# Performance work log

Hardware: AMD Instinct MI355X
Metric: run time of the kernel (lower is better)

The kernel has to match this reference:

```python
import jax, jax.numpy as jnp
import numpy as np

NEG_SLOPE = 0.2


def gat_conv(x, src, dst, W, a_src, a_dst, bias, concat, num_nodes):
    # x: [N, F_in]; W: [F_in, H*C]; a_src/a_dst: [H, C]
    H, C = a_src.shape
    h = (x @ W).reshape(num_nodes, H, C)               # [N,H,C]
    alpha_s = jnp.sum(h * a_src[None], axis=-1)        # [N,H]
    alpha_d = jnp.sum(h * a_dst[None], axis=-1)        # [N,H]
    e = jax.nn.leaky_relu(alpha_s[src] + alpha_d[dst], NEG_SLOPE)  # [E,H]
    m = jax.ops.segment_max(e, dst, num_segments=num_nodes)
    m = jnp.where(jnp.isfinite(m), m, 0.0)
    ex = jnp.exp(e - m[dst])
    denom = jax.ops.segment_sum(ex, dst, num_segments=num_nodes)
    alpha = ex / (denom[dst] + 1e-16)                  # scatter-softmax over dst
    msg = h[src] * alpha[:, :, None]                   # [E,H,C]
    out = jax.ops.segment_sum(msg, dst, num_segments=num_nodes)  # [N,H,C]
    if concat:
        out = out.reshape(num_nodes, H * C)
    else:
        out = out.mean(axis=1)
    return out + bias


def setup_inputs() -> dict:
    key = jax.random.key(0)
    ks = jax.random.split(key, 12)
    N, E = 50000, 800000
    num_concat, F_in, hid, H1, H2, n_cls = 2, 128, 64, 4, 1, 16
    x_list = jax.random.normal(ks[0], (num_concat, N, F_in), dtype=jnp.float32)
    edge_index = jax.random.randint(ks[1], (2, E), 0, N, dtype=jnp.int64)
    s = 0.1
    W1 = jax.random.normal(ks[2], (num_concat, F_in, H1 * hid), dtype=jnp.float32) * s
    att_src1 = jax.random.normal(ks[3], (num_concat, H1, hid), dtype=jnp.float32) * s
    att_dst1 = jax.random.normal(ks[4], (num_concat, H1, hid), dtype=jnp.float32) * s
    bias1 = jnp.zeros((num_concat, H1 * hid), dtype=jnp.float32)
    W2 = jax.random.normal(ks[5], (hid * H1 * num_concat, H2 * n_cls), dtype=jnp.float32) * s
    att_src2 = jax.random.normal(ks[6], (H2, n_cls), dtype=jnp.float32) * s
    att_dst2 = jax.random.normal(ks[7], (H2, n_cls), dtype=jnp.float32) * s
    bias2 = jnp.zeros((n_cls,), dtype=jnp.float32)
    return {"x_list": x_list, "edge_index": edge_index,
            "W1": W1, "att_src1": att_src1, "att_dst1": att_dst1, "bias1": bias1,
            "W2": W2, "att_src2": att_src2, "att_dst2": att_dst2, "bias2": bias2}


def reference(x_list, edge_index, W1, att_src1, att_dst1, bias1, W2, att_src2, att_dst2, bias2):
    num_concat, N, _ = x_list.shape
    loop = jnp.arange(N, dtype=edge_index.dtype)
    src = jnp.concatenate([edge_index[0], loop])  # PyG add_self_loops=True
    dst = jnp.concatenate([edge_index[1], loop])
    hidden = [jax.nn.elu(gat_conv(x_list[k], src, dst, W1[k], att_src1[k], att_dst1[k],
                                  bias1[k], True, N))
              for k in range(num_concat)]
    x = jnp.concatenate(hidden, axis=-1)           # [N, hid*H1*num_concat]
    out = gat_conv(x, src, dst, W2, att_src2, att_dst2, bias2, False, N)
    return out
```

## Files before the change

kernel.cpp:

```cpp
#include <hip/hip_runtime.h>

#define LEAKY(v) ((v) >= 0.0f ? (v) : 0.2f * (v))

typedef __attribute__((ext_vector_type(8))) short bf16x8;
typedef __attribute__((ext_vector_type(4))) float f32x4;

__device__ __forceinline__ unsigned short f2bf(float f) {
    unsigned int u = __float_as_uint(f);
    unsigned int r = u + 0x7FFFu + ((u >> 16) & 1u);
    return (unsigned short)(r >> 16);
}
__device__ __forceinline__ float bf2f(unsigned short u) {
    return __uint_as_float(((unsigned int)u) << 16);
}
__device__ __forceinline__ unsigned int pk2(float a, float b) {
    return (unsigned int)f2bf(a) | ((unsigned int)f2bf(b) << 16);
}


__global__ __launch_bounds__(256) void count_deg(const int* ei, int* deg, int E, int Etot) {
    int i = blockIdx.x * 256 + threadIdx.x;
    if (i >= Etot) return;
    int d = (i < E) ? ei[E + i] : (i - E);
    atomicAdd(&deg[d], 1);
}

__global__ __launch_bounds__(512) void scan_block(const int* deg, int* excl, int* bsum, int n) {
    __shared__ int s[512];
    int t = threadIdx.x;
    int i = blockIdx.x * 512 + t;
    int v = (i < n) ? deg[i] : 0;
    s[t] = v;
    __syncthreads();
    for (int d = 1; d < 512; d <<= 1) {
        int x = 0;
        if (t >= d) x = s[t - d];
        __syncthreads();
        if (t >= d) s[t] += x;
        __syncthreads();
    }
    if (i < n) excl[i] = s[t] - v;
    if (t == 511) bsum[blockIdx.x] = s[511];
}

__global__ __launch_bounds__(512) void scan_sums(const int* bsum, int* boff, int nb) {
    __shared__ int s[512];
    int t = threadIdx.x;
    int v = (t < nb) ? bsum[t] : 0;
    s[t] = v;
    __syncthreads();
    for (int d = 1; d < 512; d <<= 1) {
        int x = 0;
        if (t >= d) x = s[t - d];
        __syncthreads();
        if (t >= d) s[t] += x;
        __syncthreads();
    }
    boff[t] = s[t] - v;
}

__global__ __launch_bounds__(256) void finalize_off(int* csr, int* cursor, const int* boff, int n, int etot) {
    int i = blockIdx.x * 256 + threadIdx.x;
    if (i < n) {
        int v = csr[i] + boff[i >> 9];
        csr[i] = v;
        cursor[i] = v;
    }
    if (i == 0) csr[n] = etot;
}

__global__ __launch_bounds__(256) void scatter_edge(const int* ei, int* cursor, int* srcs, int* dsts,
                                                    int E, int Etot) {
    int i = blockIdx.x * 256 + threadIdx.x;
    if (i >= Etot) return;
    int s, d;
    if (i < E) { s = ei[i]; d = ei[E + i]; }
    else       { s = i - E; d = s; }
    int pos = atomicAdd(&cursor[d], 1);
    srcs[pos] = s;
    dsts[pos] = d;
}


__global__ __launch_bounds__(256) void xpack(const float* __restrict__ x, unsigned short* __restrict__ xp,
                                             int nrows) {
    int id = blockIdx.x * 256 + threadIdx.x;
    if (id >= nrows * 16) return;
    int row = id >> 4, q = id & 15;
    const float* src = x + (size_t)row * 128 + q * 8;
    float4 a = *(const float4*)src;
    float4 b = *(const float4*)(src + 4);
    uint4 v;
    v.x = pk2(a.x, a.y); v.y = pk2(a.z, a.w);
    v.z = pk2(b.x, b.y); v.w = pk2(b.z, b.w);
    *(uint4*)(xp + (size_t)row * 128 + ((q ^ (row & 7)) << 3)) = v;
}

__global__ __launch_bounds__(256) void wpack1(const float* __restrict__ W1, unsigned short* __restrict__ wt1) {
    int id = blockIdx.x * 256 + threadIdx.x;
    if (id >= 8192) return;
    int conv = id >> 12, rem = id & 4095;
    int c = rem >> 4, q = rem & 15;
    const float* src = W1 + (size_t)conv * 32768 + (size_t)(q * 8) * 256 + c;
    float w[8];
#pragma unroll
    for (int j = 0; j < 8; ++j) w[j] = src[j * 256];
    uint4 v;
    v.x = pk2(w[0], w[1]); v.y = pk2(w[2], w[3]);
    v.z = pk2(w[4], w[5]); v.w = pk2(w[6], w[7]);
    *(uint4*)(wt1 + (size_t)conv * 32768 + c * 128 + ((q ^ (c & 7)) << 3)) = v;
}

__global__ __launch_bounds__(256) void wpack2(const float* __restrict__ W2, unsigned short* __restrict__ wt2) {
    int id = blockIdx.x * 256 + threadIdx.x;
    if (id >= 1024) return;
    int s = id >> 6, l = id & 63;
    const float* src = W2 + (size_t)(s * 32 + (l >> 4) * 8) * 16 + (l & 15);
    float w[8];
#pragma unroll
    for (int j = 0; j < 8; ++j) w[j] = src[j * 16];
    uint4 v;
    v.x = pk2(w[0], w[1]); v.y = pk2(w[2], w[3]);
    v.z = pk2(w[4], w[5]); v.w = pk2(w[6], w[7]);
    *(uint4*)(wt2 + (size_t)id * 8) = v;
}


__global__ __launch_bounds__(256) void gemm1_mfma(const unsigned short* __restrict__ xp,
                                                  const unsigned short* __restrict__ wt1,
                                                  const float* __restrict__ asw, const float* __restrict__ adw,
                                                  unsigned short* __restrict__ hp,
                                                  float* __restrict__ as1, float* __restrict__ ad1, int N) {
    __shared__ unsigned short As[64 * 128];
    __shared__ unsigned short Ws[256 * 128];
    int conv = blockIdx.y;
    int t = threadIdx.x;
    int w = t >> 6, l = t & 63;

    const uint4* xsrc = (const uint4*)(xp + ((size_t)conv * N + (size_t)blockIdx.x * 64) * 128);
#pragma unroll
    for (int p = 0; p < 4; ++p) {
        int id = p * 256 + t;
        int row = id >> 4;
        int grow = blockIdx.x * 64 + row;
        uint4 v = make_uint4(0, 0, 0, 0);
        if (grow < N) v = xsrc[id];
        *(uint4*)(As + (size_t)id * 8) = v;
    }
    const uint4* wsrc = (const uint4*)(wt1 + (size_t)conv * 32768);
#pragma unroll
    for (int p = 0; p < 16; ++p) {
        int id = p * 256 + t;
        *(uint4*)(Ws + (size_t)id * 8) = wsrc[id];
    }
    __syncthreads();

    f32x4 acc[4][4];
#pragma unroll
    for (int mt = 0; mt < 4; ++mt)
#pragma unroll
        for (int nt = 0; nt < 4; ++nt) acc[mt][nt] = (f32x4){0.f, 0.f, 0.f, 0.f};

    int lr = l & 15, lg = l >> 4;
#pragma unroll
    for (int s = 0; s < 4; ++s) {
        int kq = s * 4 + lg;
        bf16x8 af[4], bf[4];
#pragma unroll
        for (int mt = 0; mt < 4; ++mt) {
            int r = mt * 16 + lr;
            af[mt] = *(const bf16x8*)(As + r * 128 + ((kq ^ (r & 7)) << 3));
        }
#pragma unroll
        for (int nt = 0; nt < 4; ++nt) {
            int c = w * 64 + nt * 16 + lr;
            bf[nt] = *(const bf16x8*)(Ws + c * 128 + ((kq ^ (c & 7)) << 3));
        }
#pragma unroll
        for (int mt = 0; mt < 4; ++mt)
#pragma unroll
            for (int nt = 0; nt < 4; ++nt)
                acc[mt][nt] = __builtin_amdgcn_mfma_f32_16x16x32_bf16(af[mt], bf[nt], acc[mt][nt], 0, 0, 0);
    }

    float aswv[4], adwv[4];
#pragma unroll
    for (int nt = 0; nt < 4; ++nt) {
        aswv[nt] = asw[conv * 256 + w * 64 + nt * 16 + lr];
        adwv[nt] = adw[conv * 256 + w * 64 + nt * 16 + lr];
    }
#pragma unroll
    for (int mt = 0; mt < 4; ++mt) {
#pragma unroll
        for (int i = 0; i < 4; ++i) {
            int grow = blockIdx.x * 64 + mt * 16 + lg * 4 + i;
            bool ok = grow < N;
            float sv = 0.f, dv = 0.f;
#pragma unroll
            for (int nt = 0; nt < 4; ++nt) {
                float hv = acc[mt][nt][i];
                if (ok) hp[(size_t)grow * 512 + (nt * 16 + lr) * 8 + conv * 4 + w] = f2bf(hv);
                sv += hv * aswv[nt];
                dv += hv * adwv[nt];
            }
#pragma unroll
            for (int o = 1; o < 16; o <<= 1) {
                sv += __shfl_xor(sv, o);
                dv += __shfl_xor(dv, o);
            }
            if (lr == 0 && ok) {
                as1[(size_t)conv * N * 4 + (size_t)grow * 4 + w] = sv;
                ad1[(size_t)conv * N * 4 + (size_t)grow * 4 + w] = dv;
            }
        }
    }
}


__global__ __launch_bounds__(256) void edge_w1(const int* __restrict__ srcs, const int* __restrict__ dsts,
                                               const float* __restrict__ as, const float* __restrict__ ad,
                                               float* __restrict__ pw, int Etot, int N4) {
    int e = blockIdx.x * 256 + threadIdx.x;
    if (e >= Etot) return;
    int s = srcs[e], d = dsts[e];
    float4 a0 = *(const float4*)(as + (size_t)s * 4);
    float4 b0 = *(const float4*)(ad + (size_t)d * 4);
    float4 a1 = *(const float4*)(as + N4 + (size_t)s * 4);
    float4 b1 = *(const float4*)(ad + N4 + (size_t)d * 4);
    float4 p0, p1;
    p0.x = __expf(LEAKY(a0.x + b0.x));
    p0.y = __expf(LEAKY(a0.y + b0.y));
    p0.z = __expf(LEAKY(a0.z + b0.z));
    p0.w = __expf(LEAKY(a0.w + b0.w));
    p1.x = __expf(LEAKY(a1.x + b1.x));
    p1.y = __expf(LEAKY(a1.y + b1.y));
    p1.z = __expf(LEAKY(a1.z + b1.z));
    p1.w = __expf(LEAKY(a1.w + b1.w));
    *(float4*)(pw + (size_t)e * 8)     = p0;
    *(float4*)(pw + (size_t)e * 8 + 4) = p1;
}


#define ACC8(g, pa, pb) {                                                      \
    float h0 = __uint_as_float((g).x << 16), h1 = __uint_as_float((g).x & 0xFFFF0000u); \
    float h2v = __uint_as_float((g).y << 16), h3 = __uint_as_float((g).y & 0xFFFF0000u); \
    float h4 = __uint_as_float((g).z << 16), h5 = __uint_as_float((g).z & 0xFFFF0000u); \
    float h6 = __uint_as_float((g).w << 16), h7 = __uint_as_float((g).w & 0xFFFF0000u); \
    den[0] += (pa).x; acc[0] += (pa).x * h0;                                   \
    den[1] += (pa).y; acc[1] += (pa).y * h1;                                   \
    den[2] += (pa).z; acc[2] += (pa).z * h2v;                                  \
    den[3] += (pa).w; acc[3] += (pa).w * h3;                                   \
    den[4] += (pb).x; acc[4] += (pb).x * h4;                                   \
    den[5] += (pb).y; acc[5] += (pb).y * h5;                                   \
    den[6] += (pb).z; acc[6] += (pb).z * h6;                                   \
    den[7] += (pb).w; acc[7] += (pb).w * h7; }

__global__ __launch_bounds__(256) void agg1_both(const unsigned short* __restrict__ hp,
                                                 const float* __restrict__ pw,
                                                 const int* __restrict__ off, const int* __restrict__ srcs,
                                                 const float* __restrict__ b1,
                                                 unsigned short* __restrict__ x2, int N) {
    int n = blockIdx.x * 4 + (threadIdx.x >> 6);
    int lane = threadIdx.x & 63;
    if (n >= N) return;
    int r0 = off[n], r1 = off[n + 1];

    float acc[8] = {0.f, 0.f, 0.f, 0.f, 0.f, 0.f, 0.f, 0.f};
    float den[8] = {0.f, 0.f, 0.f, 0.f, 0.f, 0.f, 0.f, 0.f};

    for (int base = r0; base < r1; base += 64) {
        int cnt = min(64, r1 - base);
        int my = (base + lane < r1) ? srcs[base + lane] : 0;
        int j = 0;
        for (; j + 2 <= cnt; j += 2) {
            int s0 = __shfl(my, j);
            int s1 = __shfl(my, j + 1);
            uint4 g0 = *(const uint4*)(hp + (size_t)s0 * 512 + lane * 8);
            uint4 g1 = *(const uint4*)(hp + (size_t)s1 * 512 + lane * 8);
            float4 pa0 = *(const float4*)(pw + (size_t)(base + j) * 8);
            float4 pb0 = *(const float4*)(pw + (size_t)(base + j) * 8 + 4);
            float4 pa1 = *(const float4*)(pw + (size_t)(base + j + 1) * 8);
            float4 pb1 = *(const float4*)(pw + (size_t)(base + j + 1) * 8 + 4);
            ACC8(g0, pa0, pb0);
            ACC8(g1, pa1, pb1);
        }
        if (j < cnt) {
            int s0 = __shfl(my, j);
            uint4 g0 = *(const uint4*)(hp + (size_t)s0 * 512 + lane * 8);
            float4 pa0 = *(const float4*)(pw + (size_t)(base + j) * 8);
            float4 pb0 = *(const float4*)(pw + (size_t)(base + j) * 8 + 4);
            ACC8(g0, pa0, pb0);
        }
    }

    unsigned short* xo = x2 + (size_t)n * 512;
#pragma unroll
    for (int q = 0; q < 8; ++q) {
        int k = q >> 2, hd = q & 3;
        int ofs = k * 256 + hd * 64 + lane;
        float o = acc[q] / (den[q] + 1e-16f) + b1[ofs];
        o = o > 0.f ? o : (__expf(o) - 1.0f);
        xo[ofs] = f2bf(o);
    }
}


__global__ __launch_bounds__(256) void gemm2_mfma(const unsigned short* __restrict__ x2,
                                                  const unsigned short* __restrict__ wt2,
                                                  const float* __restrict__ asw2, const float* __restrict__ adw2,
                                                  float* __restrict__ h2,
                                                  float* __restrict__ as2, float* __restrict__ ad2, int N) {
    int t = threadIdx.x;
    int w = t >> 6, l = t & 63;
    int rowbase = (blockIdx.x * 4 + w) * 16;
    if (rowbase >= N) return;
    int lr = l & 15, lg = l >> 4;

    f32x4 acc = (f32x4){0.f, 0.f, 0.f, 0.f};
    const unsigned short* ap = x2 + (size_t)(rowbase + lr) * 512 + lg * 8;
#pragma unroll
    for (int s = 0; s < 16; ++s) {
        bf16x8 av = *(const bf16x8*)(ap + s * 32);
        bf16x8 bv = *(const bf16x8*)(wt2 + ((size_t)s * 64 + l) * 8);
        acc = __builtin_amdgcn_mfma_f32_16x16x32_bf16(av, bv, acc, 0, 0, 0);
    }

    float asv = asw2[lr], adv = adw2[lr];
#pragma unroll
    for (int i = 0; i < 4; ++i) {
        int row = rowbase + lg * 4 + i;
        if (row < N) h2[(size_t)row * 16 + lr] = acc[i];
        float sv = acc[i] * asv, dv = acc[i] * adv;
#pragma unroll
        for (int o = 1; o < 16; o <<= 1) {
            sv += __shfl_xor(sv, o);
            dv += __shfl_xor(dv, o);
        }
        if (lr == 0 && row < N) { as2[row] = sv; ad2[row] = dv; }
    }
}


__global__ __launch_bounds__(256) void edge_w2(const int* __restrict__ srcs, const int* __restrict__ dsts,
                                               const float* __restrict__ as2, const float* __restrict__ ad2,
                                               float* __restrict__ p2, int Etot) {
    int e = blockIdx.x * 256 + threadIdx.x;
    if (e >= Etot) return;
    float v = as2[srcs[e]] + ad2[dsts[e]];
    p2[e] = __expf(LEAKY(v));
}


__global__ __launch_bounds__(256) void agg2(const float* __restrict__ h2,
                                            const float* __restrict__ p2,
                                            const int* __restrict__ off, const int* __restrict__ srcs,
                                            const float* __restrict__ bias2, float* __restrict__ out, int N) {
    int n = blockIdx.x * 4 + (threadIdx.x >> 6);
    int lane = threadIdx.x & 63;
    if (n >= N) return;
    int r0 = off[n], r1 = off[n + 1];

    int c = lane & 15, q = lane >> 4;
    float acc = 0.f, denom = 0.f;
    for (int e = r0 + q; e < r1; e += 4) {
        int s = srcs[e];
        float p = p2[e];
        denom += p;
        acc += p * h2[(size_t)s * 16 + c];
    }
    acc += __shfl_xor(acc, 16);     acc += __shfl_xor(acc, 32);
    denom += __shfl_xor(denom, 16); denom += __shfl_xor(denom, 32);
    if (lane < 16) out[(size_t)n * 16 + c] = acc / (denom + 1e-16f) + bias2[c];
}


extern "C" void kernel_launch(void* const* d_in, const int* in_sizes, int n_in,
                              void* d_out, int out_size, void* d_ws, size_t ws_size,
                              hipStream_t stream) {
    const float* x_list = (const float*)d_in[0];
    const int*   ei     = (const int*)d_in[1];
    const float* W1     = (const float*)d_in[2];
    const float* as1w   = (const float*)d_in[3];
    const float* ad1w   = (const float*)d_in[4];
    const float* b1     = (const float*)d_in[5];
    const float* W2     = (const float*)d_in[6];
    const float* as2w   = (const float*)d_in[7];
    const float* ad2w   = (const float*)d_in[8];
    const float* b2     = (const float*)d_in[9];
    float* out = (float*)d_out;

    const int N = in_sizes[0] / 256;
    const int E = in_sizes[1] / 2;
    const int Etot = E + N;
    const int N4 = N * 4;

    char* ws = (char*)d_ws;
    size_t woff = 0;
    auto alloc = [&](size_t bytes) {
        char* p = ws + woff;
        woff = (woff + bytes + 255) & ~(size_t)255;
        return p;
    };
    int*   csr    = (int*)alloc((size_t)(N + 1) * 4);
    int*   cursor = (int*)alloc((size_t)N * 4);
    int*   srcs   = (int*)alloc((size_t)Etot * 4);
    int*   dsts   = (int*)alloc((size_t)Etot * 4);
    int*   bsum   = (int*)alloc(512 * 4);
    int*   boff   = (int*)alloc(512 * 4);
    float* as1    = (float*)alloc((size_t)N4 * 2 * 4);
    float* ad1    = (float*)alloc((size_t)N4 * 2 * 4);
    float* as2    = (float*)alloc((size_t)N * 4);
    float* ad2    = (float*)alloc((size_t)N * 4);
    unsigned short* xp  = (unsigned short*)alloc((size_t)N * 128 * 2 * 2);
    unsigned short* wt1 = (unsigned short*)alloc(2 * 32768 * 2);
    unsigned short* wt2 = (unsigned short*)alloc(16 * 64 * 8 * 2);
    unsigned short* hp  = (unsigned short*)alloc((size_t)N * 512 * 2);
    unsigned short* x2  = (unsigned short*)alloc((size_t)N * 512 * 2);
    float* h2     = (float*)alloc((size_t)N * 16 * 4);
    float* pw     = (float*)alloc((size_t)Etot * 8 * 4);
    float* p2     = (float*)alloc((size_t)Etot * 4);

    hipMemsetAsync(cursor, 0, (size_t)N * 4, stream);
    int gE = (Etot + 255) / 256;
    count_deg<<<gE, 256, 0, stream>>>(ei, cursor, E, Etot);
    int nb = (N + 511) / 512;
    scan_block<<<nb, 512, 0, stream>>>(cursor, csr, bsum, N);
    scan_sums<<<1, 512, 0, stream>>>(bsum, boff, nb);
    finalize_off<<<(N + 255) / 256, 256, 0, stream>>>(csr, cursor, boff, N, Etot);
    scatter_edge<<<gE, 256, 0, stream>>>(ei, cursor, srcs, dsts, E, Etot);

    for (int k = 0; k < 2; ++k)
        xpack<<<(N * 16 + 255) / 256, 256, 0, stream>>>(x_list + (size_t)k * N * 128,
                                                        xp + (size_t)k * N * 128, N);
    wpack1<<<32, 256, 0, stream>>>(W1, wt1);
    wpack2<<<4, 256, 0, stream>>>(W2, wt2);

    gemm1_mfma<<<dim3((N + 63) / 64, 2), 256, 0, stream>>>(xp, wt1, as1w, ad1w, hp, as1, ad1, N);
    edge_w1<<<gE, 256, 0, stream>>>(srcs, dsts, as1, ad1, pw, Etot, N4);
    agg1_both<<<(N + 3) / 4, 256, 0, stream>>>(hp, pw, csr, srcs, b1, x2, N);

    gemm2_mfma<<<(N + 63) / 64, 256, 0, stream>>>(x2, wt2, as2w, ad2w, h2, as2, ad2, N);
    edge_w2<<<gE, 256, 0, stream>>>(srcs, dsts, as2, ad2, p2, Etot);
    agg2<<<(N + 3) / 4, 256, 0, stream>>>(h2, p2, csr, srcs, b2, out, N);
}
```

Measured before the change: 354.1 us.

## Fuse edge-weight computation into aggregation and bf16 packing into GEMM1

Drops the separate edge_w1/edge_w2 kernels and the per-edge weight buffers (and the dsts array). Attention logits are now recomputed per edge inside the aggregation kernels, using the destination's value held in a register. The x-to-bf16 packing is folded into gemm1's shared-memory load, and the hidden features are re-laid out per conv so that layer-1 aggregation runs as 8 channel slices per node, launched once per conv. This removes large intermediate writes and reads, at the cost of redundant exp computation across slices and more, smaller gathers.

Result: slower. 674.0 us (+90.4%).

```diff
diff --git a/kernel.cpp b/kernel.cpp
--- a/kernel.cpp
+++ b/kernel.cpp
@@ -16,6 +16,8 @@
 __device__ __forceinline__ unsigned int pk2(float a, float b) {
     return (unsigned int)f2bf(a) | ((unsigned int)f2bf(b) << 16);
 }
+__device__ __forceinline__ float lo16(unsigned int u) { return __uint_as_float(u << 16); }
+__device__ __forceinline__ float hi16(unsigned int u) { return __uint_as_float(u & 0xFFFF0000u); }
 
 
 __global__ __launch_bounds__(256) void count_deg(const int* ei, int* deg, int E, int Etot) {
@@ -69,8 +71,7 @@
     if (i == 0) csr[n] = etot;
 }
 
-__global__ __launch_bounds__(256) void scatter_edge(const int* ei, int* cursor, int* srcs, int* dsts,
-                                                    int E, int Etot) {
+__global__ __launch_bounds__(256) void scatter_src(const int* ei, int* cursor, int* srcs, int E, int Etot) {
     int i = blockIdx.x * 256 + threadIdx.x;
     if (i >= Etot) return;
     int s, d;
@@ -78,23 +79,8 @@
     else       { s = i - E; d = s; }
     int pos = atomicAdd(&cursor[d], 1);
     srcs[pos] = s;
-    dsts[pos] = d;
-}
-
-
-__global__ __launch_bounds__(256) void xpack(const float* __restrict__ x, unsigned short* __restrict__ xp,
-                                             int nrows) {
-    int id = blockIdx.x * 256 + threadIdx.x;
-    if (id >= nrows * 16) return;
-    int row = id >> 4, q = id & 15;
-    const float* src = x + (size_t)row * 128 + q * 8;
-    float4 a = *(const float4*)src;
-    float4 b = *(const float4*)(src + 4);
-    uint4 v;
-    v.x = pk2(a.x, a.y); v.y = pk2(a.z, a.w);
-    v.z = pk2(b.x, b.y); v.w = pk2(b.z, b.w);
-    *(uint4*)(xp + (size_t)row * 128 + ((q ^ (row & 7)) << 3)) = v;
-}
+}
+
 
 __global__ __launch_bounds__(256) void wpack1(const float* __restrict__ W1, unsigned short* __restrict__ wt1) {
     int id = blockIdx.x * 256 + threadIdx.x;
@@ -126,7 +112,7 @@
 }
 
 
-__global__ __launch_bounds__(256) void gemm1_mfma(const unsigned short* __restrict__ xp,
+__global__ __launch_bounds__(256) void gemm1_mfma(const float* __restrict__ x_list,
                                                   const unsigned short* __restrict__ wt1,
                                                   const float* __restrict__ asw, const float* __restrict__ adw,
                                                   unsigned short* __restrict__ hp,
@@ -137,15 +123,21 @@
     int t = threadIdx.x;
     int w = t >> 6, l = t & 63;
 
-    const uint4* xsrc = (const uint4*)(xp + ((size_t)conv * N + (size_t)blockIdx.x * 64) * 128);
+    const float* xg = x_list + (size_t)conv * N * 128;
 #pragma unroll
     for (int p = 0; p < 4; ++p) {
         int id = p * 256 + t;
-        int row = id >> 4;
+        int row = id >> 4, q = id & 15;
         int grow = blockIdx.x * 64 + row;
         uint4 v = make_uint4(0, 0, 0, 0);
-        if (grow < N) v = xsrc[id];
-        *(uint4*)(As + (size_t)id * 8) = v;
+        if (grow < N) {
+            const float* src = xg + (size_t)grow * 128 + q * 8;
+            float4 a = *(const float4*)src;
+            float4 b = *(const float4*)(src + 4);
+            v.x = pk2(a.x, a.y); v.y = pk2(a.z, a.w);
+            v.z = pk2(b.x, b.y); v.w = pk2(b.z, b.w);
+        }
+        *(uint4*)(As + row * 128 + ((q ^ (row & 7)) << 3)) = v;
     }
     const uint4* wsrc = (const uint4*)(wt1 + (size_t)conv * 32768);
 #pragma unroll
@@ -199,7 +191,7 @@
 #pragma unroll
             for (int nt = 0; nt < 4; ++nt) {
                 float hv = acc[mt][nt][i];
-                if (ok) hp[(size_t)grow * 512 + (nt * 16 + lr) * 8 + conv * 4 + w] = f2bf(hv);
+                if (ok) hp[((size_t)conv * N + grow) * 256 + (nt * 16 + lr) * 4 + w] = f2bf(hv);
                 sv += hv * aswv[nt];
                 dv += hv * adwv[nt];
             }
@@ -209,98 +201,67 @@
                 dv += __shfl_xor(dv, o);
             }
             if (lr == 0 && ok) {
-                as1[(size_t)conv * N * 4 + (size_t)grow * 4 + w] = sv;
-                ad1[(size_t)conv * N * 4 + (size_t)grow * 4 + w] = dv;
+                as1[((size_t)conv * N + grow) * 4 + w] = sv;
+                ad1[((size_t)conv * N + grow) * 4 + w] = dv;
             }
         }
     }
 }
 
 
-__global__ __launch_bounds__(256) void edge_w1(const int* __restrict__ srcs, const int* __restrict__ dsts,
-                                               const float* __restrict__ as, const float* __restrict__ ad,
-                                               float* __restrict__ pw, int Etot, int N4) {
-    int e = blockIdx.x * 256 + threadIdx.x;
-    if (e >= Etot) return;
-    int s = srcs[e], d = dsts[e];
-    float4 a0 = *(const float4*)(as + (size_t)s * 4);
-    float4 b0 = *(const float4*)(ad + (size_t)d * 4);
-    float4 a1 = *(const float4*)(as + N4 + (size_t)s * 4);
-    float4 b1 = *(const float4*)(ad + N4 + (size_t)d * 4);
-    float4 p0, p1;
-    p0.x = __expf(LEAKY(a0.x + b0.x));
-    p0.y = __expf(LEAKY(a0.y + b0.y));
-    p0.z = __expf(LEAKY(a0.z + b0.z));
-    p0.w = __expf(LEAKY(a0.w + b0.w));
-    p1.x = __expf(LEAKY(a1.x + b1.x));
-    p1.y = __expf(LEAKY(a1.y + b1.y));
-    p1.z = __expf(LEAKY(a1.z + b1.z));
-    p1.w = __expf(LEAKY(a1.w + b1.w));
-    *(float4*)(pw + (size_t)e * 8)     = p0;
-    *(float4*)(pw + (size_t)e * 8 + 4) = p1;
-}
-
-
-#define ACC8(g, pa, pb) {                                                      \
-    float h0 = __uint_as_float((g).x << 16), h1 = __uint_as_float((g).x & 0xFFFF0000u); \
-    float h2v = __uint_as_float((g).y << 16), h3 = __uint_as_float((g).y & 0xFFFF0000u); \
-    float h4 = __uint_as_float((g).z << 16), h5 = __uint_as_float((g).z & 0xFFFF0000u); \
-    float h6 = __uint_as_float((g).w << 16), h7 = __uint_as_float((g).w & 0xFFFF0000u); \
-    den[0] += (pa).x; acc[0] += (pa).x * h0;                                   \
-    den[1] += (pa).y; acc[1] += (pa).y * h1;                                   \
-    den[2] += (pa).z; acc[2] += (pa).z * h2v;                                  \
-    den[3] += (pa).w; acc[3] += (pa).w * h3;                                   \
-    den[4] += (pb).x; acc[4] += (pb).x * h4;                                   \
-    den[5] += (pb).y; acc[5] += (pb).y * h5;                                   \
-    den[6] += (pb).z; acc[6] += (pb).z * h6;                                   \
-    den[7] += (pb).w; acc[7] += (pb).w * h7; }
-
-__global__ __launch_bounds__(256) void agg1_both(const unsigned short* __restrict__ hp,
-                                                 const float* __restrict__ pw,
-                                                 const int* __restrict__ off, const int* __restrict__ srcs,
-                                                 const float* __restrict__ b1,
-                                                 unsigned short* __restrict__ x2, int N) {
-    int n = blockIdx.x * 4 + (threadIdx.x >> 6);
+__global__ __launch_bounds__(256) void agg1_slice(const unsigned short* __restrict__ hpk,
+                                                  const float* __restrict__ as1k, const float* __restrict__ ad1k,
+                                                  const int* __restrict__ off, const int* __restrict__ srcs,
+                                                  const float* __restrict__ b1k,
+                                                  unsigned short* __restrict__ x2, int conv, int N) {
+    int slice = blockIdx.x & 7;
+    int n = (blockIdx.x >> 3) * 4 + (threadIdx.x >> 6);
+    if (n >= N) return;
     int lane = threadIdx.x & 63;
-    if (n >= N) return;
+    int eo = lane >> 2, ci = lane & 3;
     int r0 = off[n], r1 = off[n + 1];
 
+    float4 adn = *(const float4*)(ad1k + (size_t)n * 4);
+
     float acc[8] = {0.f, 0.f, 0.f, 0.f, 0.f, 0.f, 0.f, 0.f};
-    float den[8] = {0.f, 0.f, 0.f, 0.f, 0.f, 0.f, 0.f, 0.f};
-
-    for (int base = r0; base < r1; base += 64) {
-        int cnt = min(64, r1 - base);
-        int my = (base + lane < r1) ? srcs[base + lane] : 0;
-        int j = 0;
-        for (; j + 2 <= cnt; j += 2) {
-            int s0 = __shfl(my, j);
-            int s1 = __shfl(my, j + 1);
-            uint4 g0 = *(const uint4*)(hp + (size_t)s0 * 512 + lane * 8);
-            uint4 g1 = *(const uint4*)(hp + (size_t)s1 * 512 + lane * 8);
-            float4 pa0 = *(const float4*)(pw + (size_t)(base + j) * 8);
-            float4 pb0 = *(const float4*)(pw + (size_t)(base + j) * 8 + 4);
-            float4 pa1 = *(const float4*)(pw + (size_t)(base + j + 1) * 8);
-            float4 pb1 = *(const float4*)(pw + (size_t)(base + j + 1) * 8 + 4);
-            ACC8(g0, pa0, pb0);
-            ACC8(g1, pa1, pb1);
-        }
-        if (j < cnt) {
-            int s0 = __shfl(my, j);
-            uint4 g0 = *(const uint4*)(hp + (size_t)s0 * 512 + lane * 8);
-            float4 pa0 = *(const float4*)(pw + (size_t)(base + j) * 8);
-            float4 pb0 = *(const float4*)(pw + (size_t)(base + j) * 8 + 4);
-            ACC8(g0, pa0, pb0);
-        }
-    }
-
-    unsigned short* xo = x2 + (size_t)n * 512;
-#pragma unroll
-    for (int q = 0; q < 8; ++q) {
-        int k = q >> 2, hd = q & 3;
-        int ofs = k * 256 + hd * 64 + lane;
-        float o = acc[q] / (den[q] + 1e-16f) + b1[ofs];
-        o = o > 0.f ? o : (__expf(o) - 1.0f);
-        xo[ofs] = f2bf(o);
+    float den[4] = {0.f, 0.f, 0.f, 0.f};
+
+    for (int base = r0; base + eo < r1; base += 16) {
+        int e = base + eo;
+        int s = __builtin_nontemporal_load(srcs + e);
+        float4 av = *(const float4*)(as1k + (size_t)s * 4);
+        uint4 g = *(const uint4*)(hpk + (size_t)s * 256 + slice * 32 + ci * 8);
+        float p0 = __expf(LEAKY(av.x + adn.x));
+        float p1 = __expf(LEAKY(av.y + adn.y));
+        float p2 = __expf(LEAKY(av.z + adn.z));
+        float p3 = __expf(LEAKY(av.w + adn.w));
+        den[0] += p0; den[1] += p1; den[2] += p2; den[3] += p3;
+        acc[0] += p0 * lo16(g.x); acc[1] += p1 * hi16(g.x);
+        acc[2] += p2 * lo16(g.y); acc[3] += p3 * hi16(g.y);
+        acc[4] += p0 * lo16(g.z); acc[5] += p1 * hi16(g.z);
+        acc[6] += p2 * lo16(g.w); acc[7] += p3 * hi16(g.w);
+    }
+
+#pragma unroll
+    for (int o = 4; o < 64; o <<= 1) {
+#pragma unroll
+        for (int j = 0; j < 8; ++j) acc[j] += __shfl_xor(acc[j], o);
+#pragma unroll
+        for (int j = 0; j < 4; ++j) den[j] += __shfl_xor(den[j], o);
+    }
+
+    if (eo == 0) {
+        unsigned short* xo = x2 + (size_t)n * 512 + conv * 256;
+#pragma unroll
+        for (int c2 = 0; c2 < 2; ++c2) {
+            int c = slice * 8 + ci * 2 + c2;
+#pragma unroll
+            for (int h = 0; h < 4; ++h) {
+                float o = acc[c2 * 4 + h] / (den[h] + 1e-16f) + b1k[h * 64 + c];
+                o = o > 0.f ? o : (__expf(o) - 1.0f);
+                xo[h * 64 + c] = f2bf(o);
+            }
+        }
     }
 }
 
@@ -341,30 +302,21 @@
 }
 
 
-__global__ __launch_bounds__(256) void edge_w2(const int* __restrict__ srcs, const int* __restrict__ dsts,
-                                               const float* __restrict__ as2, const float* __restrict__ ad2,
-                                               float* __restrict__ p2, int Etot) {
-    int e = blockIdx.x * 256 + threadIdx.x;
-    if (e >= Etot) return;
-    float v = as2[srcs[e]] + ad2[dsts[e]];
-    p2[e] = __expf(LEAKY(v));
-}
-
-
 __global__ __launch_bounds__(256) void agg2(const float* __restrict__ h2,
-                                            const float* __restrict__ p2,
+                                            const float* __restrict__ as2, const float* __restrict__ ad2,
                                             const int* __restrict__ off, const int* __restrict__ srcs,
                                             const float* __restrict__ bias2, float* __restrict__ out, int N) {
     int n = blockIdx.x * 4 + (threadIdx.x >> 6);
     int lane = threadIdx.x & 63;
     if (n >= N) return;
     int r0 = off[n], r1 = off[n + 1];
+    float adn = ad2[n];
 
     int c = lane & 15, q = lane >> 4;
     float acc = 0.f, denom = 0.f;
     for (int e = r0 + q; e < r1; e += 4) {
-        int s = srcs[e];
-        float p = p2[e];
+        int s = __builtin_nontemporal_load(srcs + e);
+        float p = __expf(LEAKY(as2[s] + adn));
         denom += p;
         acc += p * h2[(size_t)s * 16 + c];
     }
@@ -392,7 +344,6 @@
     const int N = in_sizes[0] / 256;
     const int E = in_sizes[1] / 2;
     const int Etot = E + N;
-    const int N4 = N * 4;
 
     char* ws = (char*)d_ws;
     size_t woff = 0;
@@ -404,21 +355,17 @@
     int*   csr    = (int*)alloc((size_t)(N + 1) * 4);
     int*   cursor = (int*)alloc((size_t)N * 4);
     int*   srcs   = (int*)alloc((size_t)Etot * 4);
-    int*   dsts   = (int*)alloc((size_t)Etot * 4);
     int*   bsum   = (int*)alloc(512 * 4);
     int*   boff   = (int*)alloc(512 * 4);
-    float* as1    = (float*)alloc((size_t)N4 * 2 * 4);
-    float* ad1    = (float*)alloc((size_t)N4 * 2 * 4);
+    float* as1    = (float*)alloc((size_t)N * 4 * 2 * 4);
+    float* ad1    = (float*)alloc((size_t)N * 4 * 2 * 4);
     float* as2    = (float*)alloc((size_t)N * 4);
     float* ad2    = (float*)alloc((size_t)N * 4);
-    unsigned short* xp  = (unsigned short*)alloc((size_t)N * 128 * 2 * 2);
     unsigned short* wt1 = (unsigned short*)alloc(2 * 32768 * 2);
     unsigned short* wt2 = (unsigned short*)alloc(16 * 64 * 8 * 2);
-    unsigned short* hp  = (unsigned short*)alloc((size_t)N * 512 * 2);
+    unsigned short* hp  = (unsigned short*)alloc((size_t)N * 256 * 2 * 2);
     unsigned short* x2  = (unsigned short*)alloc((size_t)N * 512 * 2);
     float* h2     = (float*)alloc((size_t)N * 16 * 4);
-    float* pw     = (float*)alloc((size_t)Etot * 8 * 4);
-    float* p2     = (float*)alloc((size_t)Etot * 4);
 
     hipMemsetAsync(cursor, 0, (size_t)N * 4, stream);
     int gE = (Etot + 255) / 256;
@@ -427,19 +374,18 @@
     scan_block<<<nb, 512, 0, stream>>>(cursor, csr, bsum, N);
     scan_sums<<<1, 512, 0, stream>>>(bsum, boff, nb);
     finalize_off<<<(N + 255) / 256, 256, 0, stream>>>(csr, cursor, boff, N, Etot);
-    scatter_edge<<<gE, 256, 0, stream>>>(ei, cursor, srcs, dsts, E, Etot);
-
-    for (int k = 0; k < 2; ++k)
-        xpack<<<(N * 16 + 255) / 256, 256, 0, stream>>>(x_list + (size_t)k * N * 128,
-                                                        xp + (size_t)k * N * 128, N);
+    scatter_src<<<gE, 256, 0, stream>>>(ei, cursor, srcs, E, Etot);
+
     wpack1<<<32, 256, 0, stream>>>(W1, wt1);
     wpack2<<<4, 256, 0, stream>>>(W2, wt2);
 
-    gemm1_mfma<<<dim3((N + 63) / 64, 2), 256, 0, stream>>>(xp, wt1, as1w, ad1w, hp, as1, ad1, N);
-    edge_w1<<<gE, 256, 0, stream>>>(srcs, dsts, as1, ad1, pw, Etot, N4);
-    agg1_both<<<(N + 3) / 4, 256, 0, stream>>>(hp, pw, csr, srcs, b1, x2, N);
+    gemm1_mfma<<<dim3((N + 63) / 64, 2), 256, 0, stream>>>(x_list, wt1, as1w, ad1w, hp, as1, ad1, N);
+    int gAgg = 8 * ((N + 3) / 4);
+    for (int k = 0; k < 2; ++k)
+        agg1_slice<<<gAgg, 256, 0, stream>>>(hp + (size_t)k * N * 256,
+                                             as1 + (size_t)k * N * 4, ad1 + (size_t)k * N * 4,
+                                             csr, srcs, b1 + k * 256, x2, k, N);
 
     gemm2_mfma<<<(N + 63) / 64, 256, 0, stream>>>(x2, wt2, as2w, ad2w, h2, as2, ad2, N);
-    edge_w2<<<gE, 256, 0, stream>>>(srcs, dsts, as2, ad2, p2, Etot);
-    agg2<<<(N + 3) / 4, 256, 0, stream>>>(h2, p2, csr, srcs, b2, out, N);
-}
+    agg2<<<(N + 3) / 4, 256, 0, stream>>>(h2, as2, ad2, csr, srcs, b2, out, N);
+}
```
